# Performance work log

Hardware: AMD Instinct MI355X
Metric: run time of the kernel (lower is better)

The kernel has to match this reference:

```python
import jax, jax.numpy as jnp
import numpy as np

N = 200_000      # n_reflns
NIMG = 500       # n_images
DMETA = 24       # metadata features
WIDTH = 32       # mlp_width
HID = 64         # hidden_units = 2*width (FeedForward default)
DEPTH = 20       # mlp_depth
NPOST = 2        # Normal posterior: (loc, scale)
EPS = 1e-12
KLW = 0.01       # scaling_kl_weight


def setup_inputs() -> dict:
    key = jax.random.key(0)
    ks = jax.random.split(key, 10)
    metadata = jax.random.normal(ks[0], (N, DMETA), jnp.float32)
    iobs = jax.random.normal(ks[1], (N, 1), jnp.float32)
    sigiobs = jax.random.uniform(ks[2], (N, 1), jnp.float32)
    image_ids = jnp.sort(jax.random.randint(ks[3], (N,), 0, NIMG)).astype(jnp.int32)
    n_reflns_per_image = jnp.bincount(image_ids, length=NIMG).astype(jnp.int32)
    d_img = DMETA + 2  # concat(metadata, iobs, sigiobs)
    w_img_in = jax.random.normal(ks[4], (d_img, WIDTH), jnp.float32) / np.float32(np.sqrt(d_img))
    b_img_in = jnp.zeros((WIDTH,), jnp.float32)
    w_scale_in = jax.random.normal(ks[5], (DMETA, WIDTH), jnp.float32) / np.float32(np.sqrt(DMETA))
    b_scale_in = jnp.zeros((WIDTH,), jnp.float32)
    # shared residual FeedForward stack (share_weights=True): x + W2 @ relu(W1 @ x)
    mlp_w1 = jax.random.normal(ks[6], (DEPTH, WIDTH, HID), jnp.float32) / np.float32(np.sqrt(WIDTH))
    mlp_b1 = jnp.zeros((DEPTH, HID), jnp.float32)
    mlp_w2 = jax.random.normal(ks[7], (DEPTH, HID, WIDTH), jnp.float32) * np.float32(0.1 / np.sqrt(HID))
    mlp_b2 = jnp.zeros((DEPTH, WIDTH), jnp.float32)
    w_out = jax.random.normal(ks[8], (WIDTH, NPOST), jnp.float32) / np.float32(np.sqrt(WIDTH))
    b_out = jnp.zeros((NPOST,), jnp.float32)
    return {
        'metadata': metadata, 'iobs': iobs, 'sigiobs': sigiobs,
        'w_img_in': w_img_in, 'b_img_in': b_img_in,
        'w_scale_in': w_scale_in, 'b_scale_in': b_scale_in,
        'mlp_w1': mlp_w1, 'mlp_b1': mlp_b1, 'mlp_w2': mlp_w2, 'mlp_b2': mlp_b2,
        'w_out': w_out, 'b_out': b_out,
        'image_ids_in_this_batch': image_ids,
        'n_reflns_per_image': n_reflns_per_image,
        'mc_samples': 32,
    }


def _mlp(h, w1, b1, w2, b2):
    # depth residual FF blocks, weights stacked along leading DEPTH axis
    def block(h, ws):
        wa, ba, wb, bb = ws
        h = h + (jax.nn.relu(h @ wa + ba) @ wb + bb)
        return h, None
    h, _ = jax.lax.scan(block, h, (w1, b1, w2, b2))
    return h


def reference(metadata, iobs, sigiobs,
              w_img_in, b_img_in, w_scale_in, b_scale_in,
              mlp_w1, mlp_b1, mlp_w2, mlp_b2, w_out, b_out,
              image_ids_in_this_batch, n_reflns_per_image, mc_samples):
    image = jnp.concatenate([metadata, iobs, sigiobs], axis=-1)   # (N, DMETA+2)
    h = image @ w_img_in + b_img_in                               # (N, W)
    h = _mlp(h, mlp_w1, mlp_b1, mlp_w2, mlp_b2)
    nimg = n_reflns_per_image.shape[0]
    sums = jax.ops.segment_sum(h, image_ids_in_this_batch, num_segments=nimg)
    counts = jnp.maximum(n_reflns_per_image, 1).astype(h.dtype)[:, None]
    pooled = sums / counts                                        # (NIMG, W) image-average pool
    s = metadata @ w_scale_in + b_scale_in + pooled[image_ids_in_this_batch]
    s = _mlp(s, mlp_w1, mlp_b1, mlp_w2, mlp_b2)                   # shared weights
    params = s @ w_out + b_out                                    # (N, 2)
    loc = params[:, 0]
    scale = jax.nn.softplus(params[:, 1]) + EPS
    # rsample from Normal(loc, scale), mc_samples draws
    noise = jax.random.normal(jax.random.key(42), (mc_samples, loc.shape[0]), loc.dtype)
    z = loc + scale * noise                                       # (S, N)
    # MC KL estimate: mean_s[log q(z) - log p(z)], p = Laplace(0, 1)
    log_q = -0.5 * jnp.square(noise) - jnp.log(scale) - np.float32(0.5 * np.log(2.0 * np.pi))
    log_p = -jnp.abs(z) - np.float32(np.log(2.0))
    kl_div = KLW * jnp.mean(log_q - log_p, axis=0)                # (N,)
    return z.T, kl_div
```

## Files before the change

### kernel.cpp

```cpp
#include <hip/hip_runtime.h>
#include <stdint.h>

#define N_ROWS 200000
#define NIMG   500
#define DMETA  24
#define WIDTH  32
#define HID    64
#define DEPTH  20
#define MC     32


#define WB      64000
#define LSTR2   16768
#define OFF_WI  (WB + DEPTH * LSTR2)
#define OFF_WS  (OFF_WI + 4096)
#define OFF_BIQ (OFF_WS + 4096)
#define OFF_BSQ (OFF_BIQ + 128)
#define OFF_WOQ (OFF_BSQ + 128)

typedef __attribute__((ext_vector_type(8))) short bf16x8;
typedef __attribute__((ext_vector_type(4))) float f32x4;
typedef __attribute__((ext_vector_type(16))) float f32x16;

#define MFMA32(a, b, acc) __builtin_amdgcn_mfma_f32_32x32x16_bf16((a), (b), (acc), 0, 0, 0)
#define SWP(x, y) asm("v_permlane32_swap_b32 %0, %1" : "+v"(x), "+v"(y))
#define WOFFi(h5, reg) ((((reg) & 3) + 8 * ((reg) >> 2)) + 4 * (h5))

__device__ __forceinline__ uint32_t rotl32(uint32_t x, int r) {
    return (x << r) | (x >> (32 - r));
}

__device__ __forceinline__ uint32_t tf_bits(uint32_t j) {
    const uint32_t ks1 = 42u, ks2 = 0x1BD11BDAu ^ 42u;
    uint32_t x0 = 0u, x1 = j + ks1;
#define R4(a,b,c,d) \
    x0 += x1; x1 = rotl32(x1,(a)); x1 ^= x0; \
    x0 += x1; x1 = rotl32(x1,(b)); x1 ^= x0; \
    x0 += x1; x1 = rotl32(x1,(c)); x1 ^= x0; \
    x0 += x1; x1 = rotl32(x1,(d)); x1 ^= x0;
    R4(13,15,26,6)  x0 += ks1; x1 += ks2 + 1u;
    R4(17,29,16,24) x0 += ks2; x1 += 0u + 2u;
    R4(13,15,26,6)                x1 += ks1 + 3u;
    R4(17,29,16,24) x0 += ks1; x1 += ks2 + 4u;
    R4(13,15,26,6)  x0 += ks2; x1 += 0u + 5u;
#undef R4
    return x0 ^ x1;
}

__device__ __forceinline__ float bits_to_normal(uint32_t b) {
    float f = __uint_as_float((b >> 9) | 0x3f800000u) - 1.0f;
    const float lo = -0.99999994f;
    float u = fmaxf(lo, f * 2.0f + lo);
    return 1.41421356f * erfinvf(u);
}

__device__ __forceinline__ void split1(float x, short& hi, short& lo) {
    uint32_t b = __float_as_uint(x);
    uint32_t a = b + 0x8000u;
    hi = (short)(a >> 16);
    float r = x - __uint_as_float(a & 0xFFFF0000u);
    lo = (short)(__float_as_uint(r) >> 16);
}

__device__ __forceinline__ void split8p(const float* x, bf16x8& hi, bf16x8& lo) {
    uint32_t hu[4], lu[4];
#pragma unroll
    for (int p = 0; p < 4; ++p) {
        float x0 = x[2 * p], x1 = x[2 * p + 1];
        uint32_t h;
        asm("v_cvt_pk_bf16_f32 %0, %1, %2" : "=v"(h) : "v"(x0), "v"(x1));
        float r0 = x0 - __uint_as_float(h << 16);
        float r1 = x1 - __uint_as_float(h & 0xFFFF0000u);
        uint32_t l;
        asm("v_cvt_pk_bf16_f32 %0, %1, %2" : "=v"(l) : "v"(r0), "v"(r1));
        hu[p] = h;
        lu[p] = l;
    }
    __builtin_memcpy(&hi, hu, 16);
    __builtin_memcpy(&lo, lu, 16);
}

__device__ __forceinline__ void mlp20(float* h, const char* __restrict__ wsb,
                                      int lane, int h5) {
    uint32_t lb = WB;
    const uint32_t lf = (uint32_t)(lane * 16);
#pragma unroll 1
    for (int l = 0; l < DEPTH; ++l) {
        uint32_t Hh[8], Hl[8];
#pragma unroll
        for (int p = 0; p < 8; ++p) {
            float x0 = h[2 * p], x1 = h[2 * p + 1];
            uint32_t wd;
            asm("v_cvt_pk_bf16_f32 %0, %1, %2" : "=v"(wd) : "v"(x0), "v"(x1));
            float r0 = x0 - __uint_as_float(wd << 16);
            float r1 = x1 - __uint_as_float(wd & 0xFFFF0000u);
            uint32_t ld;
            asm("v_cvt_pk_bf16_f32 %0, %1, %2" : "=v"(ld) : "v"(r0), "v"(r1));
            Hh[p] = wd;
            Hl[p] = ld;
        }
        SWP(Hh[0], Hh[2]); SWP(Hh[1], Hh[3]); SWP(Hh[4], Hh[6]); SWP(Hh[5], Hh[7]);
        SWP(Hl[0], Hl[2]); SWP(Hl[1], Hl[3]); SWP(Hl[4], Hl[6]); SWP(Hl[5], Hl[7]);
        bf16x8 B0h, B0l, B1h, B1l;
        __builtin_memcpy(&B0h, &Hh[0], 16);
        __builtin_memcpy(&B1h, &Hh[4], 16);
        __builtin_memcpy(&B0l, &Hl[0], 16);
        __builtin_memcpy(&B1l, &Hl[4], 16);
        uint32_t P[16];
#pragma unroll
        for (int tm = 0; tm < 2; ++tm) {
            f32x16 acc;
            {
                const char* bq = wsb + lb + 16384u + (uint32_t)(tm * 128 + h5 * 64);
#pragma unroll
                for (int r = 0; r < 4; ++r) {
                    f32x4 q = *(const f32x4*)(bq + 16 * r);
#pragma unroll
                    for (int i = 0; i < 4; ++i) acc[4 * r + i] = q[i];
                }
            }
            const char* fa = wsb + lb + lf + (uint32_t)(tm * 4096);
            bf16x8 a0h = *(const bf16x8*)(fa);
            bf16x8 a0l = *(const bf16x8*)(fa + 1024);
            bf16x8 a1h = *(const bf16x8*)(fa + 2048);
            bf16x8 a1l = *(const bf16x8*)(fa + 3072);
            acc = MFMA32(a0h, B0h, acc);
            acc = MFMA32(a0h, B0l, acc);
            acc = MFMA32(a0l, B0h, acc);
            acc = MFMA32(a1h, B1h, acc);
            acc = MFMA32(a1h, B1l, acc);
            acc = MFMA32(a1l, B1h, acc);
#pragma unroll
            for (int p = 0; p < 8; ++p) {
                float f0 = fmaxf(acc[2 * p], 0.0f);
                float f1 = fmaxf(acc[2 * p + 1], 0.0f);
                uint32_t wd;
                asm("v_cvt_pk_bf16_f32 %0, %1, %2" : "=v"(wd) : "v"(f0), "v"(f1));
                P[tm * 8 + p] = wd;
            }
        }
        SWP(P[0], P[2]);  SWP(P[1], P[3]);  SWP(P[4], P[6]);   SWP(P[5], P[7]);
        SWP(P[8], P[10]); SWP(P[9], P[11]); SWP(P[12], P[14]); SWP(P[13], P[15]);
        f32x16 acc2;
        {
            const char* bq = wsb + lb + 16640u + (uint32_t)(h5 * 64);
#pragma unroll
            for (int r = 0; r < 4; ++r) {
                f32x4 q = *(const f32x4*)(bq + 16 * r);
#pragma unroll
                for (int i = 0; i < 4; ++i) acc2[4 * r + i] = h[4 * r + i] + q[i];
            }
        }
#pragma unroll
        for (int ks = 0; ks < 4; ++ks) {
            bf16x8 Bk;
            __builtin_memcpy(&Bk, &P[ks * 4], 16);
            const char* fa = wsb + lb + lf + 8192u + (uint32_t)(ks * 2048);
            bf16x8 ah = *(const bf16x8*)(fa);
            bf16x8 al = *(const bf16x8*)(fa + 1024);
            acc2 = MFMA32(ah, Bk, acc2);
            acc2 = MFMA32(al, Bk, acc2);
        }
#pragma unroll
        for (int i = 0; i < 16; ++i) h[i] = acc2[i];
        lb += LSTR2;
    }
}

__device__ __forceinline__ void input_proj32(
    const bf16x8& x0h, const bf16x8& x0l, const bf16x8& x1h, const bf16x8& x1l,
    const char* __restrict__ wsb, uint32_t wfoff, uint32_t bqoff,
    float* h, int lane, int h5) {
    f32x16 acc;
    {
        const char* bq = wsb + bqoff + (uint32_t)(h5 * 64);
#pragma unroll
        for (int r = 0; r < 4; ++r) {
            f32x4 q = *(const f32x4*)(bq + 16 * r);
#pragma unroll
            for (int i = 0; i < 4; ++i) acc[4 * r + i] = q[i];
        }
    }
    const char* fa = wsb + wfoff + (uint32_t)(lane * 16);
    bf16x8 a0h = *(const bf16x8*)(fa);
    bf16x8 a0l = *(const bf16x8*)(fa + 1024);
    bf16x8 a1h = *(const bf16x8*)(fa + 2048);
    bf16x8 a1l = *(const bf16x8*)(fa + 3072);
    acc = MFMA32(a0h, x0h, acc);
    acc = MFMA32(a0h, x0l, acc);
    acc = MFMA32(a0l, x0h, acc);
    acc = MFMA32(a1h, x1h, acc);
    acc = MFMA32(a1h, x1l, acc);
    acc = MFMA32(a1l, x1h, acc);
#pragma unroll
    for (int i = 0; i < 16; ++i) h[i] = acc[i];
}

__device__ __forceinline__ void load_xfrags(
    const float* __restrict__ md, const float* __restrict__ iobs,
    const float* __restrict__ sig, int row, int h5,
    bf16x8& x0h, bf16x8& x0l, bf16x8& x1h, bf16x8& x1l) {
    float xa0[8], xa1[8];
    {
        const f32x4* rp = (const f32x4*)(md + (size_t)row * DMETA + 8 * h5);
        f32x4 a = rp[0], b = rp[1];
#pragma unroll
        for (int j = 0; j < 4; ++j) { xa0[j] = a[j]; xa0[4 + j] = b[j]; }
    }
    if (h5 == 0) {
        const f32x4* rp = (const f32x4*)(md + (size_t)row * DMETA + 16);
        f32x4 a = rp[0], b = rp[1];
#pragma unroll
        for (int j = 0; j < 4; ++j) { xa1[j] = a[j]; xa1[4 + j] = b[j]; }
    } else {
        xa1[0] = iobs ? iobs[row] : 0.0f;
        xa1[1] = sig ? sig[row] : 0.0f;
#pragma unroll
        for (int j = 2; j < 8; ++j) xa1[j] = 0.0f;
    }
    split8p(xa0, x0h, x0l);
    split8p(xa1, x1h, x1l);
}

__global__ __launch_bounds__(256) void prep_kernel(
    const float* __restrict__ w1, const float* __restrict__ w2,
    const float* __restrict__ wimg, const float* __restrict__ wsc,
    const float* __restrict__ b1, const float* __restrict__ b2,
    const float* __restrict__ bimg, const float* __restrict__ bsc,
    const float* __restrict__ wout, char* __restrict__ wsb) {
    int t = blockIdx.x * 256 + threadIdx.x;
    float* sums = (float*)wsb;
    if (t < 16000) { sums[t] = 0.0f; return; }
    t -= 16000;
    if (t < 40960) {
        int l = t >> 11, r = t & 2047;
        int tm = r >> 10, ks = (r >> 9) & 1, lane = (r >> 3) & 63, j = r & 7;
        int k = 16 * ks + 8 * (lane >> 5) + j;
        int u = 32 * tm + (lane & 31);
        short hh, ll;
        split1(w1[l * 2048 + k * 64 + u], hh, ll);
        char* base = wsb + WB + l * LSTR2 + (tm * 2 + ks) * 2048 + 2 * (lane * 8 + j);
        *(short*)base = hh;
        *(short*)(base + 1024) = ll;
        return;
    }
    t -= 40960;
    if (t < 40960) {
        int l = t >> 11, r = t & 2047;
        int ks = r >> 9, lane = (r >> 3) & 63, j = r & 7;
        int u = 16 * ks + 8 * (lane >> 5) + j;
        int w = lane & 31;
        short hh, ll;
        split1(w2[l * 2048 + u * 32 + w], hh, ll);
        char* base = wsb + WB + l * LSTR2 + 8192 + ks * 2048 + 2 * (lane * 8 + j);
        *(short*)base = hh;
        *(short*)(base + 1024) = ll;
        return;
    }
    t -= 40960;
    if (t < 1280) {
        int l = t >> 6, r = t & 63;
        int tm = r >> 5, h5 = (r >> 4) & 1, reg = r & 15;
        *(float*)(wsb + WB + l * LSTR2 + 16384 + tm * 128 + h5 * 64 + reg * 4) =
            b1[l * 64 + 32 * tm + WOFFi(h5, reg)];
        return;
    }
    t -= 1280;
    if (t < 640) {
        int l = t >> 5, r = t & 31;
        int h5 = r >> 4, reg = r & 15;
        *(float*)(wsb + WB + l * LSTR2 + 16640 + h5 * 64 + reg * 4) =
            b2[l * 32 + WOFFi(h5, reg)];
        return;
    }
    t -= 640;
    if (t < 1024) {
        int ks = t >> 9, lane = (t >> 3) & 63, j = t & 7;
        int d = 16 * ks + 8 * (lane >> 5) + j, w = lane & 31;
        float v = (d < 26) ? wimg[d * 32 + w] : 0.0f;
        short hh, ll;
        split1(v, hh, ll);
        char* base = wsb + OFF_WI + ks * 2048 + 2 * (lane * 8 + j);
        *(short*)base = hh;
        *(short*)(base + 1024) = ll;
        return;
    }
    t -= 1024;
    if (t < 1024) {
        int ks = t >> 9, lane = (t >> 3) & 63, j = t & 7;
        int d = 16 * ks + 8 * (lane >> 5) + j, w = lane & 31;
        float v = (d < 24) ? wsc[d * 32 + w] : 0.0f;
        short hh, ll;
        split1(v, hh, ll);
        char* base = wsb + OFF_WS + ks * 2048 + 2 * (lane * 8 + j);
        *(short*)base = hh;
        *(short*)(base + 1024) = ll;
        return;
    }
    t -= 1024;
    if (t < 32) {
        int h5 = t >> 4, reg = t & 15;
        *(float*)(wsb + OFF_BIQ + h5 * 64 + reg * 4) = bimg[WOFFi(h5, reg)];
        return;
    }
    t -= 32;
    if (t < 32) {
        int h5 = t >> 4, reg = t & 15;
        *(float*)(wsb + OFF_BSQ + h5 * 64 + reg * 4) = bsc[WOFFi(h5, reg)];
        return;
    }
    t -= 32;
    if (t < 64) {
        int h5 = t >> 5, r = t & 31, reg = r >> 1, comp = r & 1;
        *(float*)(wsb + OFF_WOQ + h5 * 128 + reg * 8 + comp * 4) =
            wout[WOFFi(h5, reg) * 2 + comp];
        return;
    }
}

__global__ __launch_bounds__(128, 4) void pass_a(
    const float* __restrict__ md, const float* __restrict__ iobs,
    const float* __restrict__ sig, const char* __restrict__ wsb,
    const int* __restrict__ ids, float* __restrict__ sums) {
    int lane = threadIdx.x & 63, wv = threadIdx.x >> 6;
    int h5 = lane >> 5;
    int R = (blockIdx.x * 2 + wv) * 32;
    int row = R + (lane & 31);

    bf16x8 x0h, x0l, x1h, x1l;
    load_xfrags(md, iobs, sig, row, h5, x0h, x0l, x1h, x1l);

    float h[16];
    input_proj32(x0h, x0l, x1h, x1l, wsb, OFF_WI, OFF_BIQ, h, lane, h5);
    mlp20(h, wsb, lane, h5);

    int id0 = ids[R];
    bool uni = (id0 == ids[R + 31]);
    if (uni) {
#pragma unroll
        for (int m = 1; m < 32; m <<= 1) {
#pragma unroll
            for (int i = 0; i < 16; ++i) h[i] += __shfl_xor(h[i], m, 64);
        }
        if ((lane & 31) == 0) {
#pragma unroll
            for (int i = 0; i < 16; ++i)
                atomicAdd(&sums[id0 * 32 + WOFFi(h5, i)], h[i]);
        }
    } else {
        int id = ids[row];
#pragma unroll
        for (int i = 0; i < 16; ++i)
            atomicAdd(&sums[id * 32 + WOFFi(h5, i)], h[i]);
    }
}

__global__ __launch_bounds__(256) void normalize_kernel(float* __restrict__ sums,
                                                        const int* __restrict__ cnts) {
    int t = blockIdx.x * 256 + threadIdx.x;
    if (t < NIMG * WIDTH) {
        int img = t >> 5;
        float cc = (float)max(cnts[img], 1);
        sums[t] = sums[t] / cc;
    }
}

__global__ __launch_bounds__(128, 4) void pass_b(
    const float* __restrict__ md, const char* __restrict__ wsb,
    const float* __restrict__ bout, const int* __restrict__ ids,
    const float* __restrict__ pooled, float* __restrict__ out) {
    int lane = threadIdx.x & 63, wv = threadIdx.x >> 6;
    int h5 = lane >> 5;
    int R = (blockIdx.x * 2 + wv) * 32;
    int row = R + (lane & 31);

    bf16x8 x0h, x0l, x1h, x1l;
    load_xfrags(md, nullptr, nullptr, row, h5, x0h, x0l, x1h, x1l);

    float h[16];
    input_proj32(x0h, x0l, x1h, x1l, wsb, OFF_WS, OFF_BSQ, h, lane, h5);

    {
        int idp = ids[row];
#pragma unroll
        for (int a = 0; a < 4; ++a) {
            f32x4 q = *(const f32x4*)(pooled + idp * 32 + 8 * a + 4 * h5);
#pragma unroll
            for (int i = 0; i < 4; ++i) h[4 * a + i] += q[i];
        }
    }

    mlp20(h, wsb, lane, h5);

    float p0 = 0.0f, p1 = 0.0f;
    {
        const char* wq = wsb + OFF_WOQ + (uint32_t)(h5 * 128);
#pragma unroll
        for (int r = 0; r < 8; ++r) {
            f32x4 q = *(const f32x4*)(wq + 16 * r);
            p0 = fmaf(h[2 * r], q[0], p0);
            p1 = fmaf(h[2 * r], q[1], p1);
            p0 = fmaf(h[2 * r + 1], q[2], p0);
            p1 = fmaf(h[2 * r + 1], q[3], p1);
        }
    }
    p0 += __shfl_xor(p0, 32, 64);
    p1 += __shfl_xor(p1, 32, 64);
    float loc = p0 + bout[0];
    float pb = p1 + bout[1];
    float scale = fmaxf(pb, 0.0f) + log1pf(expf(-fabsf(pb))) + 1e-12f;
    float lsg = logf(scale);

    float kp = 0.0f;
    float* zrow = out + (size_t)row * MC + h5 * 16;
#pragma unroll 4
    for (int s4 = 0; s4 < 4; ++s4) {
        f32x4 zv;
#pragma unroll
        for (int jj = 0; jj < 4; ++jj) {
            int tt = h5 * 16 + s4 * 4 + jj;
            uint32_t j = (uint32_t)(tt * N_ROWS) + (uint32_t)row;
            float n = bits_to_normal(tf_bits(j));
            float z = fmaf(scale, n, loc);
            zv[jj] = z;
            kp += fmaf(-0.5f, n * n, fabsf(z));
        }
        *(f32x4*)(zrow + s4 * 4) = zv;
    }
    kp += __shfl_xor(kp, 32, 64);
    if (h5 == 0) {
        out[(size_t)N_ROWS * MC + row] =
            0.01f * (kp * (1.0f / 32.0f) - lsg - 0.91893853320467274f + 0.69314718055994531f);
    }
}

extern "C" void kernel_launch(void* const* d_in, const int* in_sizes, int n_in,
                              void* d_out, int out_size, void* d_ws, size_t ws_size,
                              hipStream_t stream) {
    const float* md   = (const float*)d_in[0];
    const float* iobs = (const float*)d_in[1];
    const float* sig  = (const float*)d_in[2];
    const float* wimg = (const float*)d_in[3];
    const float* bimg = (const float*)d_in[4];
    const float* wsc  = (const float*)d_in[5];
    const float* bsc  = (const float*)d_in[6];
    const float* w1   = (const float*)d_in[7];
    const float* b1   = (const float*)d_in[8];
    const float* w2   = (const float*)d_in[9];
    const float* b2   = (const float*)d_in[10];
    const float* wout = (const float*)d_in[11];
    const float* bout = (const float*)d_in[12];
    const int* ids    = (const int*)d_in[13];
    const int* cnts   = (const int*)d_in[14];
    float* out = (float*)d_out;
    char* wsb = (char*)d_ws;
    float* sums = (float*)wsb;

    const int nblk = N_ROWS / 64;
    prep_kernel<<<399, 256, 0, stream>>>(w1, w2, wimg, wsc, b1, b2, bimg, bsc, wout, wsb);
    pass_a<<<nblk, 128, 0, stream>>>(md, iobs, sig, wsb, ids, sums);
    normalize_kernel<<<(NIMG * WIDTH + 255) / 256, 256, 0, stream>>>(sums, cnts);
    pass_b<<<nblk, 128, 0, stream>>>(md, wsb, bout, ids, sums, out);
}
```

Before: 401.0 us.

## Process two 32-row tiles per wavefront to reuse weight fragments across MFMAs

Each wavefront now handles 64 rows as two independent 32-row tiles and interleaves their MFMA chains. Weight and bias fragments are loaded once from the workspace and used for both tiles, which halves weight-load traffic per row. The two independent accumulators also hide MFMA dependency latency. In exchange register pressure roughly doubles, so launch bounds drop from 4 to 3 blocks per SM, and the grid is resized with a bounds check for the partial last block.

Result: faster. 391.5 us (-2.4%).

```diff
diff --git a/kernel.cpp b/kernel.cpp
--- a/kernel.cpp
+++ b/kernel.cpp
@@ -80,43 +80,52 @@
     __builtin_memcpy(&lo, lu, 16);
 }
 
-__device__ __forceinline__ void mlp20(float* h, const char* __restrict__ wsb,
-                                      int lane, int h5) {
+__device__ __forceinline__ void mkbfrag(const float* h, bf16x8* Bh, bf16x8* Bl) {
+    uint32_t Hh[8], Hl[8];
+#pragma unroll
+    for (int p = 0; p < 8; ++p) {
+        float x0 = h[2 * p], x1 = h[2 * p + 1];
+        uint32_t wd;
+        asm("v_cvt_pk_bf16_f32 %0, %1, %2" : "=v"(wd) : "v"(x0), "v"(x1));
+        float r0 = x0 - __uint_as_float(wd << 16);
+        float r1 = x1 - __uint_as_float(wd & 0xFFFF0000u);
+        uint32_t ld;
+        asm("v_cvt_pk_bf16_f32 %0, %1, %2" : "=v"(ld) : "v"(r0), "v"(r1));
+        Hh[p] = wd;
+        Hl[p] = ld;
+    }
+    SWP(Hh[0], Hh[2]); SWP(Hh[1], Hh[3]); SWP(Hh[4], Hh[6]); SWP(Hh[5], Hh[7]);
+    SWP(Hl[0], Hl[2]); SWP(Hl[1], Hl[3]); SWP(Hl[4], Hl[6]); SWP(Hl[5], Hl[7]);
+    __builtin_memcpy(&Bh[0], &Hh[0], 16);
+    __builtin_memcpy(&Bh[1], &Hh[4], 16);
+    __builtin_memcpy(&Bl[0], &Hl[0], 16);
+    __builtin_memcpy(&Bl[1], &Hl[4], 16);
+}
+
+__device__ __forceinline__ void mlp20_x2(float* h0, float* h1,
+                                         const char* __restrict__ wsb,
+                                         int lane, int h5) {
     uint32_t lb = WB;
     const uint32_t lf = (uint32_t)(lane * 16);
 #pragma unroll 1
     for (int l = 0; l < DEPTH; ++l) {
-        uint32_t Hh[8], Hl[8];
-#pragma unroll
-        for (int p = 0; p < 8; ++p) {
-            float x0 = h[2 * p], x1 = h[2 * p + 1];
-            uint32_t wd;
-            asm("v_cvt_pk_bf16_f32 %0, %1, %2" : "=v"(wd) : "v"(x0), "v"(x1));
-            float r0 = x0 - __uint_as_float(wd << 16);
-            float r1 = x1 - __uint_as_float(wd & 0xFFFF0000u);
-            uint32_t ld;
-            asm("v_cvt_pk_bf16_f32 %0, %1, %2" : "=v"(ld) : "v"(r0), "v"(r1));
-            Hh[p] = wd;
-            Hl[p] = ld;
-        }
-        SWP(Hh[0], Hh[2]); SWP(Hh[1], Hh[3]); SWP(Hh[4], Hh[6]); SWP(Hh[5], Hh[7]);
-        SWP(Hl[0], Hl[2]); SWP(Hl[1], Hl[3]); SWP(Hl[4], Hl[6]); SWP(Hl[5], Hl[7]);
-        bf16x8 B0h, B0l, B1h, B1l;
-        __builtin_memcpy(&B0h, &Hh[0], 16);
-        __builtin_memcpy(&B1h, &Hh[4], 16);
-        __builtin_memcpy(&B0l, &Hl[0], 16);
-        __builtin_memcpy(&B1l, &Hl[4], 16);
-        uint32_t P[16];
+        bf16x8 B0h[2], B0l[2], B1h[2], B1l[2];
+        mkbfrag(h0, B0h, B0l);
+        mkbfrag(h1, B1h, B1l);
+        uint32_t P0[16], P1[16];
 #pragma unroll
         for (int tm = 0; tm < 2; ++tm) {
-            f32x16 acc;
+            f32x16 acc0, acc1;
             {
                 const char* bq = wsb + lb + 16384u + (uint32_t)(tm * 128 + h5 * 64);
 #pragma unroll
                 for (int r = 0; r < 4; ++r) {
                     f32x4 q = *(const f32x4*)(bq + 16 * r);
 #pragma unroll
-                    for (int i = 0; i < 4; ++i) acc[4 * r + i] = q[i];
+                    for (int i = 0; i < 4; ++i) {
+                        acc0[4 * r + i] = q[i];
+                        acc1[4 * r + i] = q[i];
+                    }
                 }
             }
             const char* fa = wsb + lb + lf + (uint32_t)(tm * 4096);
@@ -124,61 +133,80 @@
             bf16x8 a0l = *(const bf16x8*)(fa + 1024);
             bf16x8 a1h = *(const bf16x8*)(fa + 2048);
             bf16x8 a1l = *(const bf16x8*)(fa + 3072);
-            acc = MFMA32(a0h, B0h, acc);
-            acc = MFMA32(a0h, B0l, acc);
-            acc = MFMA32(a0l, B0h, acc);
-            acc = MFMA32(a1h, B1h, acc);
-            acc = MFMA32(a1h, B1l, acc);
-            acc = MFMA32(a1l, B1h, acc);
+            acc0 = MFMA32(a0h, B0h[0], acc0);
+            acc1 = MFMA32(a0h, B1h[0], acc1);
+            acc0 = MFMA32(a0h, B0l[0], acc0);
+            acc1 = MFMA32(a0h, B1l[0], acc1);
+            acc0 = MFMA32(a0l, B0h[0], acc0);
+            acc1 = MFMA32(a0l, B1h[0], acc1);
+            acc0 = MFMA32(a1h, B0h[1], acc0);
+            acc1 = MFMA32(a1h, B1h[1], acc1);
+            acc0 = MFMA32(a1h, B0l[1], acc0);
+            acc1 = MFMA32(a1h, B1l[1], acc1);
+            acc0 = MFMA32(a1l, B0h[1], acc0);
+            acc1 = MFMA32(a1l, B1h[1], acc1);
 #pragma unroll
             for (int p = 0; p < 8; ++p) {
-                float f0 = fmaxf(acc[2 * p], 0.0f);
-                float f1 = fmaxf(acc[2 * p + 1], 0.0f);
+                float f0 = fmaxf(acc0[2 * p], 0.0f);
+                float f1 = fmaxf(acc0[2 * p + 1], 0.0f);
                 uint32_t wd;
                 asm("v_cvt_pk_bf16_f32 %0, %1, %2" : "=v"(wd) : "v"(f0), "v"(f1));
-                P[tm * 8 + p] = wd;
+                P0[tm * 8 + p] = wd;
+                float g0 = fmaxf(acc1[2 * p], 0.0f);
+                float g1 = fmaxf(acc1[2 * p + 1], 0.0f);
+                uint32_t we;
+                asm("v_cvt_pk_bf16_f32 %0, %1, %2" : "=v"(we) : "v"(g0), "v"(g1));
+                P1[tm * 8 + p] = we;
             }
         }
-        SWP(P[0], P[2]);  SWP(P[1], P[3]);  SWP(P[4], P[6]);   SWP(P[5], P[7]);
-        SWP(P[8], P[10]); SWP(P[9], P[11]); SWP(P[12], P[14]); SWP(P[13], P[15]);
-        f32x16 acc2;
+        SWP(P0[0], P0[2]);  SWP(P0[1], P0[3]);  SWP(P0[4], P0[6]);   SWP(P0[5], P0[7]);
+        SWP(P0[8], P0[10]); SWP(P0[9], P0[11]); SWP(P0[12], P0[14]); SWP(P0[13], P0[15]);
+        SWP(P1[0], P1[2]);  SWP(P1[1], P1[3]);  SWP(P1[4], P1[6]);   SWP(P1[5], P1[7]);
+        SWP(P1[8], P1[10]); SWP(P1[9], P1[11]); SWP(P1[12], P1[14]); SWP(P1[13], P1[15]);
+        f32x16 acc20, acc21;
         {
             const char* bq = wsb + lb + 16640u + (uint32_t)(h5 * 64);
 #pragma unroll
             for (int r = 0; r < 4; ++r) {
                 f32x4 q = *(const f32x4*)(bq + 16 * r);
 #pragma unroll
-                for (int i = 0; i < 4; ++i) acc2[4 * r + i] = h[4 * r + i] + q[i];
+                for (int i = 0; i < 4; ++i) {
+                    acc20[4 * r + i] = h0[4 * r + i] + q[i];
+                    acc21[4 * r + i] = h1[4 * r + i] + q[i];
+                }
             }
         }
 #pragma unroll
         for (int ks = 0; ks < 4; ++ks) {
-            bf16x8 Bk;
-            __builtin_memcpy(&Bk, &P[ks * 4], 16);
+            bf16x8 Bk0, Bk1;
+            __builtin_memcpy(&Bk0, &P0[ks * 4], 16);
+            __builtin_memcpy(&Bk1, &P1[ks * 4], 16);
             const char* fa = wsb + lb + lf + 8192u + (uint32_t)(ks * 2048);
             bf16x8 ah = *(const bf16x8*)(fa);
             bf16x8 al = *(const bf16x8*)(fa + 1024);
-            acc2 = MFMA32(ah, Bk, acc2);
-            acc2 = MFMA32(al, Bk, acc2);
-        }
-#pragma unroll
-        for (int i = 0; i < 16; ++i) h[i] = acc2[i];
+            acc20 = MFMA32(ah, Bk0, acc20);
+            acc21 = MFMA32(ah, Bk1, acc21);
+            acc20 = MFMA32(al, Bk0, acc20);
+            acc21 = MFMA32(al, Bk1, acc21);
+        }
+#pragma unroll
+        for (int i = 0; i < 16; ++i) { h0[i] = acc20[i]; h1[i] = acc21[i]; }
         lb += LSTR2;
     }
 }
 
-__device__ __forceinline__ void input_proj32(
-    const bf16x8& x0h, const bf16x8& x0l, const bf16x8& x1h, const bf16x8& x1l,
+__device__ __forceinline__ void input_proj32_x2(
+    const bf16x8* X0, const bf16x8* X1,
     const char* __restrict__ wsb, uint32_t wfoff, uint32_t bqoff,
-    float* h, int lane, int h5) {
-    f32x16 acc;
+    float* h0, float* h1, int lane, int h5) {
+    f32x16 acc0, acc1;
     {
         const char* bq = wsb + bqoff + (uint32_t)(h5 * 64);
 #pragma unroll
         for (int r = 0; r < 4; ++r) {
             f32x4 q = *(const f32x4*)(bq + 16 * r);
 #pragma unroll
-            for (int i = 0; i < 4; ++i) acc[4 * r + i] = q[i];
+            for (int i = 0; i < 4; ++i) { acc0[4 * r + i] = q[i]; acc1[4 * r + i] = q[i]; }
         }
     }
     const char* fa = wsb + wfoff + (uint32_t)(lane * 16);
@@ -186,20 +214,25 @@
     bf16x8 a0l = *(const bf16x8*)(fa + 1024);
     bf16x8 a1h = *(const bf16x8*)(fa + 2048);
     bf16x8 a1l = *(const bf16x8*)(fa + 3072);
-    acc = MFMA32(a0h, x0h, acc);
-    acc = MFMA32(a0h, x0l, acc);
-    acc = MFMA32(a0l, x0h, acc);
-    acc = MFMA32(a1h, x1h, acc);
-    acc = MFMA32(a1h, x1l, acc);
-    acc = MFMA32(a1l, x1h, acc);
-#pragma unroll
-    for (int i = 0; i < 16; ++i) h[i] = acc[i];
+    acc0 = MFMA32(a0h, X0[0], acc0);
+    acc1 = MFMA32(a0h, X1[0], acc1);
+    acc0 = MFMA32(a0h, X0[1], acc0);
+    acc1 = MFMA32(a0h, X1[1], acc1);
+    acc0 = MFMA32(a0l, X0[0], acc0);
+    acc1 = MFMA32(a0l, X1[0], acc1);
+    acc0 = MFMA32(a1h, X0[2], acc0);
+    acc1 = MFMA32(a1h, X1[2], acc1);
+    acc0 = MFMA32(a1h, X0[3], acc0);
+    acc1 = MFMA32(a1h, X1[3], acc1);
+    acc0 = MFMA32(a1l, X0[2], acc0);
+    acc1 = MFMA32(a1l, X1[2], acc1);
+#pragma unroll
+    for (int i = 0; i < 16; ++i) { h0[i] = acc0[i]; h1[i] = acc1[i]; }
 }
 
 __device__ __forceinline__ void load_xfrags(
     const float* __restrict__ md, const float* __restrict__ iobs,
-    const float* __restrict__ sig, int row, int h5,
-    bf16x8& x0h, bf16x8& x0l, bf16x8& x1h, bf16x8& x1l) {
+    const float* __restrict__ sig, int row, int h5, bf16x8* X) {
     float xa0[8], xa1[8];
     {
         const f32x4* rp = (const f32x4*)(md + (size_t)row * DMETA + 8 * h5);
@@ -218,8 +251,8 @@
 #pragma unroll
         for (int j = 2; j < 8; ++j) xa1[j] = 0.0f;
     }
-    split8p(xa0, x0h, x0l);
-    split8p(xa1, x1h, x1l);
+    split8p(xa0, X[0], X[1]);
+    split8p(xa1, X[2], X[3]);
 }
 
 __global__ __launch_bounds__(256) void prep_kernel(
@@ -318,40 +351,49 @@
     }
 }
 
-__global__ __launch_bounds__(128, 4) void pass_a(
+__global__ __launch_bounds__(128, 3) void pass_a(
     const float* __restrict__ md, const float* __restrict__ iobs,
     const float* __restrict__ sig, const char* __restrict__ wsb,
     const int* __restrict__ ids, float* __restrict__ sums) {
     int lane = threadIdx.x & 63, wv = threadIdx.x >> 6;
     int h5 = lane >> 5;
-    int R = (blockIdx.x * 2 + wv) * 32;
-    int row = R + (lane & 31);
-
-    bf16x8 x0h, x0l, x1h, x1l;
-    load_xfrags(md, iobs, sig, row, h5, x0h, x0l, x1h, x1l);
-
-    float h[16];
-    input_proj32(x0h, x0l, x1h, x1l, wsb, OFF_WI, OFF_BIQ, h, lane, h5);
-    mlp20(h, wsb, lane, h5);
-
-    int id0 = ids[R];
-    bool uni = (id0 == ids[R + 31]);
-    if (uni) {
-#pragma unroll
-        for (int m = 1; m < 32; m <<= 1) {
-#pragma unroll
-            for (int i = 0; i < 16; ++i) h[i] += __shfl_xor(h[i], m, 64);
-        }
-        if ((lane & 31) == 0) {
+    int gw = blockIdx.x * 2 + wv;
+    int R = gw * 64;
+    if (R >= N_ROWS) return;
+    int row0 = R + (lane & 31), row1 = row0 + 32;
+
+    bf16x8 X0[4], X1[4];
+    load_xfrags(md, iobs, sig, row0, h5, X0);
+    load_xfrags(md, iobs, sig, row1, h5, X1);
+
+    float h0[16], h1[16];
+    input_proj32_x2(X0, X1, wsb, OFF_WI, OFF_BIQ, h0, h1, lane, h5);
+    mlp20_x2(h0, h1, wsb, lane, h5);
+
+#pragma unroll
+    for (int tile = 0; tile < 2; ++tile) {
+        float* h = tile ? h1 : h0;
+        int tb = R + tile * 32;
+        int rowt = tile ? row1 : row0;
+        int id0 = ids[tb];
+        bool uni = (id0 == ids[tb + 31]);
+        if (uni) {
+#pragma unroll
+            for (int m = 1; m < 32; m <<= 1) {
+#pragma unroll
+                for (int i = 0; i < 16; ++i) h[i] += __shfl_xor(h[i], m, 64);
+            }
+            if ((lane & 31) == 0) {
+#pragma unroll
+                for (int i = 0; i < 16; ++i)
+                    atomicAdd(&sums[id0 * 32 + WOFFi(h5, i)], h[i]);
+            }
+        } else {
+            int id = ids[rowt];
 #pragma unroll
             for (int i = 0; i < 16; ++i)
-                atomicAdd(&sums[id0 * 32 + WOFFi(h5, i)], h[i]);
-        }
-    } else {
-        int id = ids[row];
-#pragma unroll
-        for (int i = 0; i < 16; ++i)
-            atomicAdd(&sums[id * 32 + WOFFi(h5, i)], h[i]);
+                atomicAdd(&sums[id * 32 + WOFFi(h5, i)], h[i]);
+        }
     }
 }
 
@@ -365,23 +407,28 @@
     }
 }
 
-__global__ __launch_bounds__(128, 4) void pass_b(
+__global__ __launch_bounds__(128, 3) void pass_b(
     const float* __restrict__ md, const char* __restrict__ wsb,
     const float* __restrict__ bout, const int* __restrict__ ids,
     const float* __restrict__ pooled, float* __restrict__ out) {
     int lane = threadIdx.x & 63, wv = threadIdx.x >> 6;
     int h5 = lane >> 5;
-    int R = (blockIdx.x * 2 + wv) * 32;
-    int row = R + (lane & 31);
-
-    bf16x8 x0h, x0l, x1h, x1l;
-    load_xfrags(md, nullptr, nullptr, row, h5, x0h, x0l, x1h, x1l);
-
-    float h[16];
-    input_proj32(x0h, x0l, x1h, x1l, wsb, OFF_WS, OFF_BSQ, h, lane, h5);
-
-    {
-        int idp = ids[row];
+    int gw = blockIdx.x * 2 + wv;
+    int R = gw * 64;
+    if (R >= N_ROWS) return;
+    int row0 = R + (lane & 31), row1 = row0 + 32;
+
+    bf16x8 X0[4], X1[4];
+    load_xfrags(md, nullptr, nullptr, row0, h5, X0);
+    load_xfrags(md, nullptr, nullptr, row1, h5, X1);
+
+    float h0[16], h1[16];
+    input_proj32_x2(X0, X1, wsb, OFF_WS, OFF_BSQ, h0, h1, lane, h5);
+
+#pragma unroll
+    for (int tile = 0; tile < 2; ++tile) {
+        float* h = tile ? h1 : h0;
+        int idp = ids[tile ? row1 : row0];
 #pragma unroll
         for (int a = 0; a < 4; ++a) {
             f32x4 q = *(const f32x4*)(pooled + idp * 32 + 8 * a + 4 * h5);
@@ -390,47 +437,54 @@
         }
     }
 
-    mlp20(h, wsb, lane, h5);
-
-    float p0 = 0.0f, p1 = 0.0f;
+    mlp20_x2(h0, h1, wsb, lane, h5);
+
+    f32x4 wq[8];
     {
-        const char* wq = wsb + OFF_WOQ + (uint32_t)(h5 * 128);
+        const char* wp = wsb + OFF_WOQ + (uint32_t)(h5 * 128);
+#pragma unroll
+        for (int r = 0; r < 8; ++r) wq[r] = *(const f32x4*)(wp + 16 * r);
+    }
+#pragma unroll
+    for (int tile = 0; tile < 2; ++tile) {
+        const float* h = tile ? h1 : h0;
+        int row = tile ? row1 : row0;
+        float p0 = 0.0f, p1 = 0.0f;
 #pragma unroll
         for (int r = 0; r < 8; ++r) {
-            f32x4 q = *(const f32x4*)(wq + 16 * r);
-            p0 = fmaf(h[2 * r], q[0], p0);
-            p1 = fmaf(h[2 * r], q[1], p1);
-            p0 = fmaf(h[2 * r + 1], q[2], p0);
-            p1 = fmaf(h[2 * r + 1], q[3], p1);
-        }
-    }
-    p0 += __shfl_xor(p0, 32, 64);
-    p1 += __shfl_xor(p1, 32, 64);
-    float loc = p0 + bout[0];
-    float pb = p1 + bout[1];
-    float scale = fmaxf(pb, 0.0f) + log1pf(expf(-fabsf(pb))) + 1e-12f;
-    float lsg = logf(scale);
-
-    float kp = 0.0f;
-    float* zrow = out + (size_t)row * MC + h5 * 16;
+            p0 = fmaf(h[2 * r], wq[r][0], p0);
+            p1 = fmaf(h[2 * r], wq[r][1], p1);
+            p0 = fmaf(h[2 * r + 1], wq[r][2], p0);
+            p1 = fmaf(h[2 * r + 1], wq[r][3], p1);
+        }
+        p0 += __shfl_xor(p0, 32, 64);
+        p1 += __shfl_xor(p1, 32, 64);
+        float loc = p0 + bout[0];
+        float pb = p1 + bout[1];
+        float scale = fmaxf(pb, 0.0f) + log1pf(expf(-fabsf(pb))) + 1e-12f;
+        float lsg = logf(scale);
+
+        float kp = 0.0f;
+        float* zrow = out + (size_t)row * MC + h5 * 16;
 #pragma unroll 4
-    for (int s4 = 0; s4 < 4; ++s4) {
-        f32x4 zv;
-#pragma unroll
-        for (int jj = 0; jj < 4; ++jj) {
-            int tt = h5 * 16 + s4 * 4 + jj;
-            uint32_t j = (uint32_t)(tt * N_ROWS) + (uint32_t)row;
-            float n = bits_to_normal(tf_bits(j));
-            float z = fmaf(scale, n, loc);
-            zv[jj] = z;
-            kp += fmaf(-0.5f, n * n, fabsf(z));
-        }
-        *(f32x4*)(zrow + s4 * 4) = zv;
-    }
-    kp += __shfl_xor(kp, 32, 64);
-    if (h5 == 0) {
-        out[(size_t)N_ROWS * MC + row] =
-            0.01f * (kp * (1.0f / 32.0f) - lsg - 0.91893853320467274f + 0.69314718055994531f);
+        for (int s4 = 0; s4 < 4; ++s4) {
+            f32x4 zv;
+#pragma unroll
+            for (int jj = 0; jj < 4; ++jj) {
+                int tt = h5 * 16 + s4 * 4 + jj;
+                uint32_t j = (uint32_t)(tt * N_ROWS) + (uint32_t)row;
+                float n = bits_to_normal(tf_bits(j));
+                float z = fmaf(scale, n, loc);
+                zv[jj] = z;
+                kp += fmaf(-0.5f, n * n, fabsf(z));
+            }
+            *(f32x4*)(zrow + s4 * 4) = zv;
+        }
+        kp += __shfl_xor(kp, 32, 64);
+        if (h5 == 0) {
+            out[(size_t)N_ROWS * MC + row] =
+                0.01f * (kp * (1.0f / 32.0f) - lsg - 0.91893853320467274f + 0.69314718055994531f);
+        }
     }
 }
 
@@ -456,7 +510,7 @@
     char* wsb = (char*)d_ws;
     float* sums = (float*)wsb;
 
-    const int nblk = N_ROWS / 64;
+    const int nblk = 1563;
     prep_kernel<<<399, 256, 0, stream>>>(w1, w2, wimg, wsc, b1, b2, bimg, bsc, wout, wsb);
     pass_a<<<nblk, 128, 0, stream>>>(md, iobs, sig, wsb, ids, sums);
     normalize_kernel<<<(NIMG * WIDTH + 255) / 256, 256, 0, stream>>>(sums, cnts);
```
